# Optimization experiments

Hardware: AMD Instinct MI355X
Metric: run time of the kernel (lower is better)

The kernel has to match this reference:

```python
import jax, jax.numpy as jnp
import numpy as np

D_MODEL = 1024
NUM_HEADS = 16
HEAD_DIM = D_MODEL // NUM_HEADS
SCALE = HEAD_DIM ** -0.5


def setup_inputs() -> dict:
    key = jax.random.key(0)
    ks = jax.random.split(key, 9)
    s = 1.0 / np.sqrt(D_MODEL)
    return {
        "query": jax.random.normal(ks[0], (4, 2048, D_MODEL), dtype=jnp.float32),
        "Wq": jax.random.normal(ks[1], (D_MODEL, D_MODEL), dtype=jnp.float32) * s,
        "bq": jax.random.normal(ks[2], (D_MODEL,), dtype=jnp.float32) * 0.01,
        "Wk": jax.random.normal(ks[3], (D_MODEL, D_MODEL), dtype=jnp.float32) * s,
        "bk": jax.random.normal(ks[4], (D_MODEL,), dtype=jnp.float32) * 0.01,
        "Wv": jax.random.normal(ks[5], (D_MODEL, D_MODEL), dtype=jnp.float32) * s,
        "bv": jax.random.normal(ks[6], (D_MODEL,), dtype=jnp.float32) * 0.01,
        "Wo": jax.random.normal(ks[7], (D_MODEL, D_MODEL), dtype=jnp.float32) * s,
        "bo": jax.random.normal(ks[8], (D_MODEL,), dtype=jnp.float32) * 0.01,
    }


def reference(query, Wq, bq, Wk, bk, Wv, bv, Wo, bo):
    # Self-attention (key=value=query). dropout=0, no mask, so chunked
    # computation equals full softmax attention exactly.
    b, s, d = query.shape
    q = (query @ Wq + bq).reshape(b, s, NUM_HEADS, HEAD_DIM)
    k = (query @ Wk + bk).reshape(b, s, NUM_HEADS, HEAD_DIM)
    v = (query @ Wv + bv).reshape(b, s, NUM_HEADS, HEAD_DIM)
    # scores: [b, h, s_q, s_k]
    scores = jnp.einsum("bqhd,bkhd->bhqk", q, k) * SCALE
    attn = jax.nn.softmax(scores, axis=-1)
    ctx = jnp.einsum("bhqk,bkhd->bqhd", attn, v).reshape(b, s, d)
    return ctx @ Wo + bo
```

## Files before the change

kernel.cpp:

```cpp
#include <hip/hip_runtime.h>
#include <stdint.h>

#define NHEADS 16
#define HDIM   64
#define SEQ    2048
#define BATCH  4
#define DM     1024
#define MTOT   (BATCH*SEQ)
#define SCALE  0.125f

typedef unsigned short u16;
typedef __attribute__((ext_vector_type(8))) short short8;
typedef __attribute__((ext_vector_type(4))) float f32x4;

__device__ __forceinline__ u16 f2bf(float f) {
  uint32_t u = __builtin_bit_cast(uint32_t, f);
  u += 0x7FFFu + ((u >> 16) & 1u);
  return (u16)(u >> 16);
}

__device__ __forceinline__ f32x4 mfma16(short8 a, short8 b, f32x4 c) {
  return __builtin_amdgcn_mfma_f32_16x16x32_bf16(a, b, c, 0, 0, 0);
}

__device__ __forceinline__ void gload16(const u16* g, u16* l) {
  __builtin_amdgcn_global_load_lds((const __attribute__((address_space(1))) void*)g,
                                   (__attribute__((address_space(3))) void*)l,
                                   16, 0, 0);
}

#define LDSP(base, row, boff) \
  ((u16*)((char*)(base) + (((row) << 7) + ((boff) ^ (((row) & 7) << 4)))))

__global__ __launch_bounds__(256) void k_conv(const float* __restrict__ in, u16* __restrict__ out) {
  size_t i = (size_t)blockIdx.x * 256 + threadIdx.x;
  const float4* p = (const float4*)(in + i * 8);
  float4 a = p[0], b = p[1];
  u16 r[8] = {f2bf(a.x), f2bf(a.y), f2bf(a.z), f2bf(a.w),
              f2bf(b.x), f2bf(b.y), f2bf(b.z), f2bf(b.w)};
  *(short8*)(out + i * 8) = *(const short8*)r;
}

__global__ __launch_bounds__(256) void k_convw(const float* __restrict__ w0, const float* __restrict__ w1,
                                               const float* __restrict__ w2, const float* __restrict__ w3,
                                               u16* __restrict__ o0, u16* __restrict__ o1,
                                               u16* __restrict__ o2, u16* __restrict__ o3) {
  const float* W = blockIdx.z==0?w0: blockIdx.z==1?w1: blockIdx.z==2?w2:w3;
  u16* O        = blockIdx.z==0?o0: blockIdx.z==1?o1: blockIdx.z==2?o2:o3;
  __shared__ float tile[32][33];
  int t = threadIdx.x;
  int k0 = blockIdx.y*32, n0 = blockIdx.x*32;
  int r = t >> 5, c = t & 31;
  #pragma unroll
  for (int p = 0; p < 4; ++p) tile[r + 8*p][c] = W[(size_t)(k0 + r + 8*p)*DM + n0 + c];
  __syncthreads();
  #pragma unroll
  for (int p = 0; p < 4; ++p) O[(size_t)(n0 + r + 8*p)*DM + k0 + c] = f2bf(tile[c][r + 8*p]);
}

template<int MODE>
__global__ __launch_bounds__(256) void k_gemm(
    const u16* __restrict__ A,
    const u16* __restrict__ WtQ, const u16* __restrict__ WtK, const u16* __restrict__ WtV,
    const float* __restrict__ bQ, const float* __restrict__ bK, const float* __restrict__ bV,
    u16* __restrict__ oQ, u16* __restrict__ oK, u16* __restrict__ oV,
    float* __restrict__ oF)
{
  __shared__ u16 As[128*32];
  __shared__ u16 Bs[128*32];
  const int t = threadIdx.x;
  const int lane = t & 63;
  const int lo = lane & 15, q4 = lane >> 4;
  const int w  = t >> 6, wm = w >> 1, wn = w & 1;

  int m0, n0, z;
  if (MODE == 0) {
    int L = blockIdx.x + 8 * blockIdx.y + 512 * blockIdx.z;
    int work = (L & 7) * 192 + (L >> 3);
    z  = work % 3;
    n0 = ((work / 3) & 7) * 128;
    m0 = (work / 24) * 128;
  } else {
    int L = blockIdx.x + 8 * blockIdx.y;
    int work = (L & 7) * 64 + (L >> 3);
    z  = 0;
    n0 = (work & 7) * 128;
    m0 = (work >> 3) * 128;
  }

  const u16* Wt; const float* bias;
  if (MODE == 0) {
    Wt   = (z==0)?WtQ:(z==1)?WtK:WtV;
    bias = (z==0)?bQ:(z==1)?bK:bV;
  } else { Wt = WtQ; bias = bQ; }

  f32x4 acc[4][4] = {};

  const int gr = lane >> 2;
  const int gc = (lane & 3) * 8;

  for (int kt = 0; kt < 32; ++kt) {
    const int k0 = kt * 32;
    __syncthreads();
    gload16(A  + (size_t)(m0 + w*32 +  0 + gr)*DM + k0 + gc, As + (w*32 +  0)*32);
    gload16(A  + (size_t)(m0 + w*32 + 16 + gr)*DM + k0 + gc, As + (w*32 + 16)*32);
    gload16(Wt + (size_t)(n0 + w*32 +  0 + gr)*DM + k0 + gc, Bs + (w*32 +  0)*32);
    gload16(Wt + (size_t)(n0 + w*32 + 16 + gr)*DM + k0 + gc, Bs + (w*32 + 16)*32);
    __syncthreads();

    short8 af[4], bf[4];
    #pragma unroll
    for (int i = 0; i < 4; ++i)
      af[i] = *(const short8*)(As + (wm*64 + i*16 + lo)*32 + q4*8);
    #pragma unroll
    for (int i = 0; i < 4; ++i)
      bf[i] = *(const short8*)(Bs + (wn*64 + i*16 + lo)*32 + q4*8);
    #pragma unroll
    for (int i = 0; i < 4; ++i)
      #pragma unroll
      for (int j = 0; j < 4; ++j)
        acc[i][j] = mfma16(af[i], bf[j], acc[i][j]);
  }

  #pragma unroll
  for (int i = 0; i < 4; ++i) {
    #pragma unroll
    for (int j = 0; j < 4; ++j) {
      int col = n0 + wn*64 + j*16 + lo;
      float bvv = bias[col];
      #pragma unroll
      for (int r = 0; r < 4; ++r) {
        int row = m0 + wm*64 + i*16 + q4*4 + r;
        float v = acc[i][j][r] + bvv;
        if (MODE == 0) {
          int b = row >> 11, s = row & 2047, h = col >> 6, d = col & 63;
          if (z == 2) oV[(size_t)((b*16 + h)*64 + d)*SEQ + s] = f2bf(v);
          else if (z == 0) oQ[(size_t)((b*16 + h)*SEQ + s)*HDIM + d] = f2bf(v * SCALE);
          else             oK[(size_t)((b*16 + h)*SEQ + s)*HDIM + d] = f2bf(v);
        } else {
          oF[(size_t)row*DM + col] = v;
        }
      }
    }
  }
}

__global__ __launch_bounds__(256, 4) void k_attn(
    const u16* __restrict__ Q,
    const u16* __restrict__ K,
    const u16* __restrict__ VT,
    u16* __restrict__ O)
{
  __shared__ u16 Ks[64*64];
  __shared__ u16 Vs[64*64];
  __shared__ u16 Ps[4][2][16*64];
  const int t = threadIdx.x, lane = t & 63, w = t >> 6;
  const int lo = lane & 15, q4 = lane >> 4;
  const int bh = blockIdx.x, qt = blockIdx.y;
  const int qbase = qt*128 + w*32;

  const u16* Qp = Q  + ((size_t)bh * SEQ + qbase) * HDIM;
  const u16* Kp = K  + (size_t)bh * SEQ * HDIM;
  const u16* Vp = VT + (size_t)bh * HDIM * SEQ;

  short8 qf[2][2];
  #pragma unroll
  for (int g = 0; g < 2; ++g)
    #pragma unroll
    for (int kd = 0; kd < 2; ++kd)
      qf[g][kd] = *(const short8*)(Qp + (size_t)(g*16 + lo)*HDIM + kd*32 + q4*8);

  f32x4 acc[2][4] = {};
  float m_run[2] = {-3.0e38f, -3.0e38f};
  float l_run[2] = {0.f, 0.f};

  const int sr = t >> 3;
  const int sc = t & 7;
  short8 kr0 = *(const short8*)(Kp + (size_t)(sr     )*HDIM + sc*8);
  short8 kr1 = *(const short8*)(Kp + (size_t)(sr + 32)*HDIM + sc*8);
  short8 vr0 = *(const short8*)(Vp + (size_t)(sr     )*SEQ  + sc*8);
  short8 vr1 = *(const short8*)(Vp + (size_t)(sr + 32)*SEQ  + sc*8);

  u16* PsW = &Ps[w][0][0];

  for (int kt = 0; kt < 32; ++kt) {
    __syncthreads();
    *(short8*)LDSP(Ks, sr,      sc*16) = kr0;
    *(short8*)LDSP(Ks, sr + 32, sc*16) = kr1;
    *(short8*)LDSP(Vs, sr,      sc*16) = vr0;
    *(short8*)LDSP(Vs, sr + 32, sc*16) = vr1;
    {
      int kn = (kt + 1 < 32) ? kt + 1 : 31;
      kr0 = *(const short8*)(Kp + (size_t)(kn*64 + sr     )*HDIM + sc*8);
      kr1 = *(const short8*)(Kp + (size_t)(kn*64 + sr + 32)*HDIM + sc*8);
      vr0 = *(const short8*)(Vp + (size_t)(sr     )*SEQ + kn*64 + sc*8);
      vr1 = *(const short8*)(Vp + (size_t)(sr + 32)*SEQ + kn*64 + sc*8);
    }
    __syncthreads();

    #pragma unroll
    for (int g = 0; g < 2; ++g) {
      f32x4 sv[4];
      #pragma unroll
      for (int fc = 0; fc < 4; ++fc) {
        short8 k0 = *(const short8*)LDSP(Ks, fc*16 + lo,      q4*16);
        short8 k1 = *(const short8*)LDSP(Ks, fc*16 + lo, 64 + q4*16);
        f32x4 z = {};
        z = mfma16(k0, qf[g][0], z);
        z = mfma16(k1, qf[g][1], z);
        sv[fc] = z;
      }
      float mx = fmaxf(fmaxf(fmaxf(sv[0][0], sv[0][1]), fmaxf(sv[0][2], sv[0][3])),
                       fmaxf(fmaxf(sv[1][0], sv[1][1]), fmaxf(sv[1][2], sv[1][3])));
      mx = fmaxf(mx, fmaxf(fmaxf(fmaxf(sv[2][0], sv[2][1]), fmaxf(sv[2][2], sv[2][3])),
                           fmaxf(fmaxf(sv[3][0], sv[3][1]), fmaxf(sv[3][2], sv[3][3]))));
      mx = fmaxf(mx, __shfl_xor(mx, 16));
      mx = fmaxf(mx, __shfl_xor(mx, 32));
      if (__any(mx > m_run[g] + 8.f)) {
        float mn = fmaxf(m_run[g], mx);
        float al = __expf(m_run[g] - mn);
        m_run[g] = mn;
        l_run[g] *= al;
        f32x4 av;
        av[0] = __shfl(al, q4*4 + 0); av[1] = __shfl(al, q4*4 + 1);
        av[2] = __shfl(al, q4*4 + 2); av[3] = __shfl(al, q4*4 + 3);
        #pragma unroll
        for (int fd = 0; fd < 4; ++fd) acc[g][fd] *= av;
      }
      float sum = 0.f;
      u16* PsG = PsW + g*(16*64);
      #pragma unroll
      for (int fc = 0; fc < 4; ++fc) {
        uint32_t u0 = __builtin_bit_cast(uint32_t, __expf(sv[fc][0] - m_run[g]));
        uint32_t u1 = __builtin_bit_cast(uint32_t, __expf(sv[fc][1] - m_run[g]));
        uint32_t u2 = __builtin_bit_cast(uint32_t, __expf(sv[fc][2] - m_run[g]));
        uint32_t u3 = __builtin_bit_cast(uint32_t, __expf(sv[fc][3] - m_run[g]));
        sum += __builtin_bit_cast(float, u0 & 0xffff0000u)
             + __builtin_bit_cast(float, u1 & 0xffff0000u)
             + __builtin_bit_cast(float, u2 & 0xffff0000u)
             + __builtin_bit_cast(float, u3 & 0xffff0000u);
        uint2 pk;
        pk.x = (u0 >> 16) | (u1 & 0xffff0000u);
        pk.y = (u2 >> 16) | (u3 & 0xffff0000u);
        *(uint2*)LDSP(PsG, lo, fc*32 + q4*8) = pk;
      }
      sum += __shfl_xor(sum, 16);
      sum += __shfl_xor(sum, 32);
      l_run[g] += sum;
    }

    #pragma unroll
    for (int ks = 0; ks < 2; ++ks) {
      short8 pa0 = *(const short8*)LDSP(PsW,         lo, ks*64 + q4*16);
      short8 pa1 = *(const short8*)LDSP(PsW + 16*64, lo, ks*64 + q4*16);
      #pragma unroll
      for (int fd = 0; fd < 4; ++fd) {
        short8 vf = *(const short8*)LDSP(Vs, fd*16 + lo, ks*64 + q4*16);
        acc[0][fd] = mfma16(pa0, vf, acc[0][fd]);
        acc[1][fd] = mfma16(pa1, vf, acc[1][fd]);
      }
    }
  }

  const int b = bh >> 4, h = bh & 15;
  #pragma unroll
  for (int g = 0; g < 2; ++g) {
    f32x4 inv;
    inv[0] = 1.f / __shfl(l_run[g], q4*4 + 0);
    inv[1] = 1.f / __shfl(l_run[g], q4*4 + 1);
    inv[2] = 1.f / __shfl(l_run[g], q4*4 + 2);
    inv[3] = 1.f / __shfl(l_run[g], q4*4 + 3);
    #pragma unroll
    for (int fd = 0; fd < 4; ++fd)
      #pragma unroll
      for (int r = 0; r < 4; ++r) {
        int qg = qbase + g*16 + q4*4 + r;
        O[((size_t)(b*SEQ + qg)*NHEADS + h)*HDIM + fd*16 + lo] = f2bf(acc[g][fd][r] * inv[r]);
      }
  }
}

extern "C" void kernel_launch(void* const* d_in, const int* in_sizes, int n_in,
                              void* d_out, int out_size, void* d_ws, size_t ws_size,
                              hipStream_t stream) {
  const float* query = (const float*)d_in[0];
  const float* Wq = (const float*)d_in[1]; const float* bq = (const float*)d_in[2];
  const float* Wk = (const float*)d_in[3]; const float* bk = (const float*)d_in[4];
  const float* Wv = (const float*)d_in[5]; const float* bv = (const float*)d_in[6];
  const float* Wo = (const float*)d_in[7]; const float* bo = (const float*)d_in[8];
  float* out = (float*)d_out;

  u16* qb  = (u16*)d_ws;
  u16* wt0 = qb  + (size_t)MTOT*DM;
  u16* wt1 = wt0 + (size_t)DM*DM;
  u16* wt2 = wt1 + (size_t)DM*DM;
  u16* wt3 = wt2 + (size_t)DM*DM;
  u16* qp  = wt3 + (size_t)DM*DM;
  u16* kp  = qp  + (size_t)MTOT*DM;
  u16* vt  = kp  + (size_t)MTOT*DM;

  k_conv<<<dim3(MTOT*DM/8/256), 256, 0, stream>>>(query, qb);
  k_convw<<<dim3(32, 32, 4), 256, 0, stream>>>(Wq, Wk, Wv, Wo, wt0, wt1, wt2, wt3);
  k_gemm<0><<<dim3(8, 64, 3), 256, 0, stream>>>(qb, wt0, wt1, wt2, bq, bk, bv, qp, kp, vt, nullptr);
  k_attn<<<dim3(64, 16), 256, 0, stream>>>(qp, kp, vt, qb );
  k_gemm<1><<<dim3(8, 64, 1), 256, 0, stream>>>(qb, wt3, nullptr, nullptr, bo, nullptr, nullptr,
                                                nullptr, nullptr, nullptr, out);
}
```

Measured before the change: 325.9 us.

## Rewrite attention with 32x32 MFMA, register-resident P via permlane swap

The attention kernel moves from 16x16x32 to 32x32x16 bf16 MFMA tiles, with 64 queries per wave and 256 per block. The P matrix stays in registers and is rearranged with permlane32_swap instead of a round trip through LDS. The softmax folds log2(e) into the Q scale so it can use exp2f, and the output is staged through LDS for coalesced 16-byte stores. The goals are fewer LDS accesses and better MFMA efficiency, at the cost of higher register pressure, fewer blocks, and lower occupancy (launch bounds drop from 4 to 2).

```diff
diff --git a/kernel.cpp b/kernel.cpp
--- a/kernel.cpp
+++ b/kernel.cpp
@@ -8,10 +8,13 @@
 #define DM     1024
 #define MTOT   (BATCH*SEQ)
 #define SCALE  0.125f
+#define QSCALE 0.18033688011112042f
 
 typedef unsigned short u16;
 typedef __attribute__((ext_vector_type(8))) short short8;
 typedef __attribute__((ext_vector_type(4))) float f32x4;
+typedef __attribute__((ext_vector_type(16))) float f32x16;
+typedef __attribute__((ext_vector_type(4))) unsigned int u32x4;
 
 __device__ __forceinline__ u16 f2bf(float f) {
   uint32_t u = __builtin_bit_cast(uint32_t, f);
@@ -21,6 +24,9 @@
 
 __device__ __forceinline__ f32x4 mfma16(short8 a, short8 b, f32x4 c) {
   return __builtin_amdgcn_mfma_f32_16x16x32_bf16(a, b, c, 0, 0, 0);
+}
+__device__ __forceinline__ f32x16 mfma32(short8 a, short8 b, f32x16 c) {
+  return __builtin_amdgcn_mfma_f32_32x32x16_bf16(a, b, c, 0, 0, 0);
 }
 
 __device__ __forceinline__ void gload16(const u16* g, u16* l) {
@@ -135,7 +141,7 @@
         if (MODE == 0) {
           int b = row >> 11, s = row & 2047, h = col >> 6, d = col & 63;
           if (z == 2) oV[(size_t)((b*16 + h)*64 + d)*SEQ + s] = f2bf(v);
-          else if (z == 0) oQ[(size_t)((b*16 + h)*SEQ + s)*HDIM + d] = f2bf(v * SCALE);
+          else if (z == 0) oQ[(size_t)((b*16 + h)*SEQ + s)*HDIM + d] = f2bf(v * QSCALE);
           else             oK[(size_t)((b*16 + h)*SEQ + s)*HDIM + d] = f2bf(v);
         } else {
           oF[(size_t)row*DM + col] = v;
@@ -145,138 +151,139 @@
   }
 }
 
-__global__ __launch_bounds__(256, 4) void k_attn(
+__global__ __launch_bounds__(256, 2) void k_attn(
     const u16* __restrict__ Q,
     const u16* __restrict__ K,
     const u16* __restrict__ VT,
     u16* __restrict__ O)
 {
-  __shared__ u16 Ks[64*64];
-  __shared__ u16 Vs[64*64];
-  __shared__ u16 Ps[4][2][16*64];
+  __shared__ u16 lds[16384];
+  u16* Ks = lds;
+  u16* Vs = lds + 4096;
   const int t = threadIdx.x, lane = t & 63, w = t >> 6;
-  const int lo = lane & 15, q4 = lane >> 4;
+  const int l31 = lane & 31, h = lane >> 5;
   const int bh = blockIdx.x, qt = blockIdx.y;
-  const int qbase = qt*128 + w*32;
-
-  const u16* Qp = Q  + ((size_t)bh * SEQ + qbase) * HDIM;
+  const int qw = qt*256 + w*64;
+
+  const u16* Qp = Q  + ((size_t)bh * SEQ + qw) * HDIM;
   const u16* Kp = K  + (size_t)bh * SEQ * HDIM;
   const u16* Vp = VT + (size_t)bh * HDIM * SEQ;
 
-  short8 qf[2][2];
+  short8 qf[2][4];
   #pragma unroll
   for (int g = 0; g < 2; ++g)
     #pragma unroll
-    for (int kd = 0; kd < 2; ++kd)
-      qf[g][kd] = *(const short8*)(Qp + (size_t)(g*16 + lo)*HDIM + kd*32 + q4*8);
-
-  f32x4 acc[2][4] = {};
-  float m_run[2] = {-3.0e38f, -3.0e38f};
+    for (int c = 0; c < 4; ++c)
+      qf[g][c] = *(const short8*)(Qp + (size_t)(g*32 + l31)*HDIM + c*16 + h*8);
+
+  f32x16 acc[2][2] = {};
+  float m_run[2] = {-1e38f, -1e38f};
   float l_run[2] = {0.f, 0.f};
 
-  const int sr = t >> 3;
-  const int sc = t & 7;
-  short8 kr0 = *(const short8*)(Kp + (size_t)(sr     )*HDIM + sc*8);
-  short8 kr1 = *(const short8*)(Kp + (size_t)(sr + 32)*HDIM + sc*8);
-  short8 vr0 = *(const short8*)(Vp + (size_t)(sr     )*SEQ  + sc*8);
-  short8 vr1 = *(const short8*)(Vp + (size_t)(sr + 32)*SEQ  + sc*8);
-
-  u16* PsW = &Ps[w][0][0];
+  const int sr = t >> 2, sc = t & 3;
+  const u16* Kg = Kp + (size_t)sr * HDIM;
+  const u16* Vg = Vp + (size_t)sr * SEQ;
+  short8 kr0 = *(const short8*)(Kg + sc*8);
+  short8 kr1 = *(const short8*)(Kg + (sc+4)*8);
+  short8 vr0 = *(const short8*)(Vg + sc*8);
+  short8 vr1 = *(const short8*)(Vg + (sc+4)*8);
 
   for (int kt = 0; kt < 32; ++kt) {
     __syncthreads();
-    *(short8*)LDSP(Ks, sr,      sc*16) = kr0;
-    *(short8*)LDSP(Ks, sr + 32, sc*16) = kr1;
-    *(short8*)LDSP(Vs, sr,      sc*16) = vr0;
-    *(short8*)LDSP(Vs, sr + 32, sc*16) = vr1;
+    *(short8*)LDSP(Ks, sr, sc*16)     = kr0;
+    *(short8*)LDSP(Ks, sr, (sc+4)*16) = kr1;
+    *(short8*)LDSP(Vs, sr, sc*16)     = vr0;
+    *(short8*)LDSP(Vs, sr, (sc+4)*16) = vr1;
     {
-      int kn = (kt + 1 < 32) ? kt + 1 : 31;
-      kr0 = *(const short8*)(Kp + (size_t)(kn*64 + sr     )*HDIM + sc*8);
-      kr1 = *(const short8*)(Kp + (size_t)(kn*64 + sr + 32)*HDIM + sc*8);
-      vr0 = *(const short8*)(Vp + (size_t)(sr     )*SEQ + kn*64 + sc*8);
-      vr1 = *(const short8*)(Vp + (size_t)(sr + 32)*SEQ + kn*64 + sc*8);
+      int kn = (kt + 1 < 32 ? kt + 1 : 31) * 64;
+      kr0 = *(const short8*)(Kg + (size_t)kn*HDIM + sc*8);
+      kr1 = *(const short8*)(Kg + (size_t)kn*HDIM + (sc+4)*8);
+      vr0 = *(const short8*)(Vg + kn + sc*8);
+      vr1 = *(const short8*)(Vg + kn + (sc+4)*8);
     }
     __syncthreads();
 
     #pragma unroll
-    for (int g = 0; g < 2; ++g) {
-      f32x4 sv[4];
-      #pragma unroll
-      for (int fc = 0; fc < 4; ++fc) {
-        short8 k0 = *(const short8*)LDSP(Ks, fc*16 + lo,      q4*16);
-        short8 k1 = *(const short8*)LDSP(Ks, fc*16 + lo, 64 + q4*16);
-        f32x4 z = {};
-        z = mfma16(k0, qf[g][0], z);
-        z = mfma16(k1, qf[g][1], z);
-        sv[fc] = z;
-      }
-      float mx = fmaxf(fmaxf(fmaxf(sv[0][0], sv[0][1]), fmaxf(sv[0][2], sv[0][3])),
-                       fmaxf(fmaxf(sv[1][0], sv[1][1]), fmaxf(sv[1][2], sv[1][3])));
-      mx = fmaxf(mx, fmaxf(fmaxf(fmaxf(sv[2][0], sv[2][1]), fmaxf(sv[2][2], sv[2][3])),
-                           fmaxf(fmaxf(sv[3][0], sv[3][1]), fmaxf(sv[3][2], sv[3][3]))));
-      mx = fmaxf(mx, __shfl_xor(mx, 16));
-      mx = fmaxf(mx, __shfl_xor(mx, 32));
-      if (__any(mx > m_run[g] + 8.f)) {
-        float mn = fmaxf(m_run[g], mx);
-        float al = __expf(m_run[g] - mn);
-        m_run[g] = mn;
-        l_run[g] *= al;
-        f32x4 av;
-        av[0] = __shfl(al, q4*4 + 0); av[1] = __shfl(al, q4*4 + 1);
-        av[2] = __shfl(al, q4*4 + 2); av[3] = __shfl(al, q4*4 + 3);
-        #pragma unroll
-        for (int fd = 0; fd < 4; ++fd) acc[g][fd] *= av;
-      }
-      float sum = 0.f;
-      u16* PsG = PsW + g*(16*64);
-      #pragma unroll
-      for (int fc = 0; fc < 4; ++fc) {
-        uint32_t u0 = __builtin_bit_cast(uint32_t, __expf(sv[fc][0] - m_run[g]));
-        uint32_t u1 = __builtin_bit_cast(uint32_t, __expf(sv[fc][1] - m_run[g]));
-        uint32_t u2 = __builtin_bit_cast(uint32_t, __expf(sv[fc][2] - m_run[g]));
-        uint32_t u3 = __builtin_bit_cast(uint32_t, __expf(sv[fc][3] - m_run[g]));
-        sum += __builtin_bit_cast(float, u0 & 0xffff0000u)
-             + __builtin_bit_cast(float, u1 & 0xffff0000u)
-             + __builtin_bit_cast(float, u2 & 0xffff0000u)
-             + __builtin_bit_cast(float, u3 & 0xffff0000u);
-        uint2 pk;
-        pk.x = (u0 >> 16) | (u1 & 0xffff0000u);
-        pk.y = (u2 >> 16) | (u3 & 0xffff0000u);
-        *(uint2*)LDSP(PsG, lo, fc*32 + q4*8) = pk;
-      }
-      sum += __shfl_xor(sum, 16);
-      sum += __shfl_xor(sum, 32);
-      l_run[g] += sum;
-    }
-
-    #pragma unroll
-    for (int ks = 0; ks < 2; ++ks) {
-      short8 pa0 = *(const short8*)LDSP(PsW,         lo, ks*64 + q4*16);
-      short8 pa1 = *(const short8*)LDSP(PsW + 16*64, lo, ks*64 + q4*16);
-      #pragma unroll
-      for (int fd = 0; fd < 4; ++fd) {
-        short8 vf = *(const short8*)LDSP(Vs, fd*16 + lo, ks*64 + q4*16);
-        acc[0][fd] = mfma16(pa0, vf, acc[0][fd]);
-        acc[1][fd] = mfma16(pa1, vf, acc[1][fd]);
+    for (int kb = 0; kb < 2; ++kb) {
+      short8 kf[4];
+      #pragma unroll
+      for (int c = 0; c < 4; ++c)
+        kf[c] = *(const short8*)LDSP(Ks, kb*32 + l31, c*32 + h*16);
+      short8 vf[2][2];
+      #pragma unroll
+      for (int dt = 0; dt < 2; ++dt)
+        #pragma unroll
+        for (int k2 = 0; k2 < 2; ++k2)
+          vf[dt][k2] = *(const short8*)LDSP(Vs, dt*32 + l31, kb*64 + k2*32 + h*16);
+
+      #pragma unroll
+      for (int g = 0; g < 2; ++g) {
+        f32x16 s = {};
+        #pragma unroll
+        for (int c = 0; c < 4; ++c) s = mfma32(kf[c], qf[g][c], s);
+
+        float mx = s[0];
+        #pragma unroll
+        for (int i = 1; i < 16; ++i) mx = fmaxf(mx, s[i]);
+        mx = fmaxf(mx, __shfl_xor(mx, 32));
+        if (__any(mx > m_run[g] + 11.5f)) {
+          float mn = fmaxf(m_run[g], mx);
+          float al = exp2f(m_run[g] - mn);
+          m_run[g] = mn;
+          l_run[g] *= al;
+          #pragma unroll
+          for (int dt = 0; dt < 2; ++dt)
+            #pragma unroll
+            for (int i = 0; i < 16; ++i) acc[g][dt][i] *= al;
+        }
+        const float pm = m_run[g];
+        float sum = 0.f;
+        uint32_t W[8];
+        #pragma unroll
+        for (int i8 = 0; i8 < 8; ++i8) {
+          float pe = exp2f(s[2*i8]   - pm);
+          float po = exp2f(s[2*i8+1] - pm);
+          sum += pe + po;
+          W[i8] = (__builtin_bit_cast(uint32_t, pe) >> 16)
+                | (__builtin_bit_cast(uint32_t, po) & 0xffff0000u);
+        }
+        sum += __shfl_xor(sum, 32);
+        l_run[g] += sum;
+
+        #pragma unroll
+        for (int k2 = 0; k2 < 2; ++k2) {
+          auto r0 = __builtin_amdgcn_permlane32_swap(W[4*k2 + 0], W[4*k2 + 2], false, false);
+          auto r1 = __builtin_amdgcn_permlane32_swap(W[4*k2 + 1], W[4*k2 + 3], false, false);
+          u32x4 pw; pw[0] = r0[0]; pw[1] = r1[0]; pw[2] = r0[1]; pw[3] = r1[1];
+          short8 pf = __builtin_bit_cast(short8, pw);
+          #pragma unroll
+          for (int dt = 0; dt < 2; ++dt)
+            acc[g][dt] = mfma32(vf[dt][k2], pf, acc[g][dt]);
+        }
       }
     }
   }
 
-  const int b = bh >> 4, h = bh & 15;
+  __syncthreads();
+  u16* ep = lds + w*4096;
   #pragma unroll
   for (int g = 0; g < 2; ++g) {
-    f32x4 inv;
-    inv[0] = 1.f / __shfl(l_run[g], q4*4 + 0);
-    inv[1] = 1.f / __shfl(l_run[g], q4*4 + 1);
-    inv[2] = 1.f / __shfl(l_run[g], q4*4 + 2);
-    inv[3] = 1.f / __shfl(l_run[g], q4*4 + 3);
-    #pragma unroll
-    for (int fd = 0; fd < 4; ++fd)
-      #pragma unroll
-      for (int r = 0; r < 4; ++r) {
-        int qg = qbase + g*16 + q4*4 + r;
-        O[((size_t)(b*SEQ + qg)*NHEADS + h)*HDIM + fd*16 + lo] = f2bf(acc[g][fd][r] * inv[r]);
+    float inv = 1.f / l_run[g];
+    #pragma unroll
+    for (int dt = 0; dt < 2; ++dt)
+      #pragma unroll
+      for (int i = 0; i < 16; ++i) {
+        int d = dt*32 + (i & 3) + 8*(i >> 2) + 4*h;
+        *LDSP(ep, g*32 + l31, 2*d) = f2bf(acc[g][dt][i] * inv);
       }
+  }
+  const int b = bh >> 4, hh = bh & 15;
+  #pragma unroll
+  for (int it = 0; it < 8; ++it) {
+    int row = it*8 + (lane >> 3);
+    int s = qw + row;
+    short8 v = *(const short8*)LDSP(ep, row, (lane & 7)*16);
+    *(short8*)(O + ((size_t)(b*SEQ + s)*NHEADS + hh)*HDIM + (lane & 7)*8) = v;
   }
 }
 
@@ -302,7 +309,7 @@
   k_conv<<<dim3(MTOT*DM/8/256), 256, 0, stream>>>(query, qb);
   k_convw<<<dim3(32, 32, 4), 256, 0, stream>>>(Wq, Wk, Wv, Wo, wt0, wt1, wt2, wt3);
   k_gemm<0><<<dim3(8, 64, 3), 256, 0, stream>>>(qb, wt0, wt1, wt2, bq, bk, bv, qp, kp, vt, nullptr);
-  k_attn<<<dim3(64, 16), 256, 0, stream>>>(qp, kp, vt, qb );
+  k_attn<<<dim3(64, 8), 256, 0, stream>>>(qp, kp, vt, qb );
   k_gemm<1><<<dim3(8, 64, 1), 256, 0, stream>>>(qb, wt3, nullptr, nullptr, bo, nullptr, nullptr,
                                                 nullptr, nullptr, nullptr, out);
 }
```

New measurement: 323.6 us. About the same (-0.7%).
